# Kernel optimization log

Hardware: AMD Instinct MI355X
Metric: run time of the kernel (lower is better)

Reference implementation:

```python
import jax, jax.numpy as jnp
import numpy as np

N, E, G = 100000, 1600000, 8
IN, H, OUT = 3, 64, 20


def setup_inputs() -> dict:
    key = jax.random.key(0)
    ks = jax.random.split(key, 24)
    def nrm(k, shape, scale=0.1):
        return jax.random.normal(k, shape, dtype=jnp.float32) * scale
    inp = {}
    inp["x"] = jax.random.normal(ks[0], (N, IN), dtype=jnp.float32)
    inp["edge_index"] = jax.random.randint(ks[1], (2, E), 0, N, dtype=jnp.int32)
    inp["batch"] = jnp.sort(jax.random.randint(ks[2], (N,), 0, G, dtype=jnp.int32))
    dims = [(IN, H), (H, H), (H, H)]  # 3 GATConv layers (initial + layers-1)
    for i, (di, do) in enumerate(dims):
        inp[f"W{i}"] = nrm(ks[3 + 4 * i], (di, do))
        inp[f"as{i}"] = nrm(ks[4 + 4 * i], (do,))
        inp[f"ad{i}"] = nrm(ks[5 + 4 * i], (do,))
        inp[f"b{i}"] = jnp.zeros((do,), jnp.float32)
    inp["vn_emb0"] = jnp.zeros((1, H), jnp.float32)  # constant-0 init per module
    inp["m1_w1"] = nrm(ks[15], (H, H)); inp["m1_b1"] = jnp.zeros((H,), jnp.float32)
    inp["m1_w2"] = nrm(ks[16], (H, H)); inp["m1_b2"] = jnp.zeros((H,), jnp.float32)
    inp["mf_w1"] = nrm(ks[17], (H, H)); inp["mf_b1"] = jnp.zeros((H,), jnp.float32)
    inp["mf_w2"] = nrm(ks[18], (H, OUT)); inp["mf_b2"] = jnp.zeros((OUT,), jnp.float32)
    inp["out_w"] = nrm(ks[19], (H, OUT)); inp["out_b"] = jnp.zeros((OUT,), jnp.float32)
    return inp


def _gat(x, src, dst, W, a_s, a_d, b):
    # PyG GATConv, 1 head: h = xW; e_ij = LeakyReLU_0.2(a_s.h_j + a_d.h_i);
    # alpha = softmax over incoming edges of each dst node; out_i = sum_j alpha_ij h_j + b
    h = x @ W                                                  # [N, H]
    lg = jax.nn.leaky_relu((h @ a_s)[src] + (h @ a_d)[dst], 0.2)  # [E+N]
    m = jax.ops.segment_max(lg, dst, num_segments=N)
    m = jnp.where(jnp.isfinite(m), m, 0.0)
    p = jnp.exp(lg - m[dst])
    denom = jax.ops.segment_sum(p, dst, num_segments=N)
    alpha = p / denom[dst]
    return jax.ops.segment_sum(alpha[:, None] * h[src], dst, num_segments=N) + b


def _forward(x, edge_index, batch, params):
    (W0, as0, ad0, b0, W1, as1, ad1, b1, W2, as2, ad2, b2,
     vn_emb0, m1_w1, m1_b1, m1_w2, m1_b2, mf_w1, mf_b1, mf_w2, mf_b2,
     out_w, out_b) = params
    loops = jnp.arange(N, dtype=edge_index.dtype)  # GATConv add_self_loops=True
    src = jnp.concatenate([edge_index[0], loops])
    dst = jnp.concatenate([edge_index[1], loops])
    act = lambda v: jax.nn.leaky_relu(v, 0.01)  # nn.LeakyReLU default slope
    h = act(_gat(x, src, dst, W0, as0, ad0, b0))
    h = act(_gat(h, src, dst, W1, as1, ad1, b1))
    h = act(_gat(h, src, dst, W2, as2, ad2, b2))
    # virtual node: global_add_pool(out, batch) + Embedding(0) (zero-init)
    vn = jax.ops.segment_sum(h, batch, num_segments=G) + vn_emb0[0]
    vn = jax.nn.relu(vn @ m1_w1 + m1_b1)
    vn = jax.nn.relu(vn @ m1_w2 + m1_b2)
    vn = jax.nn.relu(vn @ mf_w1 + mf_b1)
    vn = jax.nn.relu(vn @ mf_w2 + mf_b2)
    return (h @ out_w + out_b, vn)


def reference(x, edge_index, batch, W0, as0, ad0, b0, W1, as1, ad1, b1,
              W2, as2, ad2, b2, vn_emb0, m1_w1, m1_b1, m1_w2, m1_b2,
              mf_w1, mf_b1, mf_w2, mf_b2, out_w, out_b):
    params = (W0, as0, ad0, b0, W1, as1, ad1, b1, W2, as2, ad2, b2,
              vn_emb0, m1_w1, m1_b1, m1_w2, m1_b2, mf_w1, mf_b1, mf_w2, mf_b2,
              out_w, out_b)
    return _forward(x, edge_index, batch, params)
```

## Files before the change

kernel.cpp:

```cpp
#include <hip/hip_runtime.h>
#include <hip/hip_bf16.h>

#define H 64
#define OUTD 20
#define NGRAPH 8
#define NBK 256
#define CAPB 8192
#define MAXDEG 63

typedef __attribute__((ext_vector_type(8))) short bf16x8;
typedef __attribute__((ext_vector_type(4))) float f32x4;
typedef __attribute__((ext_vector_type(8))) unsigned short u16x8;


__device__ __forceinline__ float ldp(const void* p, int i, bool f32) {
    return f32 ? ((const float*)p)[i]
               : __bfloat162float(((const __hip_bfloat16*)p)[i]);
}

__device__ __forceinline__ float bfu(unsigned short u) {
    union { unsigned int i; float f; } c; c.i = ((unsigned)u) << 16; return c.f;
}
__device__ __forceinline__ unsigned short fbits(float f) {
    __hip_bfloat16 b = __float2bfloat16(f);
    return *reinterpret_cast<unsigned short*>(&b);
}

__global__ void detect_dtype(const unsigned short* __restrict__ xb, int n_u16,
                             int* __restrict__ flag, int* __restrict__ gcur,
                             int* __restrict__ gtot, float* __restrict__ vnp,
                             float* __restrict__ s, short* __restrict__ hbuf,
                             int n, int ns) {
    __shared__ int sh[256];
    int t = threadIdx.x;
    int m = min(n_u16, 4096);
    int bad = 0;
    for (int i = t; i < m; i += 256) {
        unsigned e = (xb[i] >> 7) & 0xFF;
        bad += (e >= 0x90) ? 1 : 0;
    }
    sh[t] = bad;
    if (t < NBK) gcur[t] = 0;
    for (int i = t; i < NGRAPH * H; i += 256) vnp[i] = 0.f;
    if (t < 32) hbuf[(size_t)n * 32 + t] = 0;
    else if (t < 64) hbuf[((size_t)ns + n) * 32 + (t - 32)] = 0;
    if (t == 0) { *gtot = 0; s[n] = -1e30f; }
    __syncthreads();
    for (int off = 128; off; off >>= 1) {
        if (t < off) sh[t] += sh[t + off];
        __syncthreads();
    }
    if (t == 0) *flag = (sh[0] > (m >> 4)) ? 1 : 0;
}

__global__ void fillC_dense0(const int* __restrict__ src, const int* __restrict__ dst,
                             int* __restrict__ gcur, unsigned* __restrict__ ebuf,
                             int E, int n, int ns, int nC, int EPC, int nbk,
                             const void* __restrict__ x, const void* __restrict__ W,
                             const void* __restrict__ a_s, const void* __restrict__ a_d,
                             __hip_bfloat16* __restrict__ h, float* __restrict__ s,
                             float* __restrict__ d, const int* __restrict__ flagp) {
    if ((int)blockIdx.x < nC) {
        __shared__ unsigned lcnt[NBK];
        __shared__ int lbase[NBK];
        int t = threadIdx.x;
        for (int i = t; i < NBK; i += 256) lcnt[i] = 0;
        __syncthreads();
        int base = blockIdx.x * (256 * EPC) + t;
        for (int i = 0; i < EPC; ++i) {
            int e = base + i * 256;
            if (e < E) {
                int dn = dst[e];
                if ((unsigned)dn < (unsigned)n) atomicAdd(&lcnt[dn >> 9], 1u);
            }
        }
        __syncthreads();
        for (int i = t; i < nbk; i += 256) {
            unsigned c = lcnt[i];
            lbase[i] = c ? atomicAdd(&gcur[i], (int)c) : 0;
            lcnt[i] = 0;
        }
        __syncthreads();
        for (int i = 0; i < EPC; ++i) {
            int e = base + i * 256;
            if (e < E) {
                int dn = dst[e];
                if ((unsigned)dn < (unsigned)n) {
                    int b = dn >> 9;
                    unsigned pos = (unsigned)lbase[b] + atomicAdd(&lcnt[b], 1u);
                    if (pos < CAPB)
                        ebuf[(size_t)b * CAPB + pos] =
                            ((unsigned)src[e] << 9) | (unsigned)(dn & 511);
                }
            }
        }
        return;
    }
    const bool f32 = (*flagp != 0);
    int idx = ((int)blockIdx.x - nC) * 256 + threadIdx.x;
    int node = idx >> 6;
    int f = idx & 63;
    if (node >= n) return;
    float acc = 0.f;
    for (int k = 0; k < 3; ++k)
        acc += ldp(x, node * 3 + k, f32) * ldp(W, k * H + f, f32);
    ((short*)h)[((size_t)(f >> 5) * ns + node) * 32 + (f & 31)] = (short)fbits(acc);
    float sv = acc * ldp(a_s, f, f32);
    float dv = acc * ldp(a_d, f, f32);
    for (int off = 32; off; off >>= 1) {
        sv += __shfl_xor(sv, off);
        dv += __shfl_xor(dv, off);
    }
    if (f == 0) { s[node] = sv; d[node] = dv; }
}

__global__ __launch_bounds__(512) void bucketD(const unsigned* __restrict__ ebuf,
                                               const int* __restrict__ gcur,
                                               unsigned* __restrict__ cntoff,
                                               int* __restrict__ col,
                                               int* __restrict__ gtot, int n) {
    __shared__ unsigned lcnt[512];
    __shared__ int loff[512];
    __shared__ int sc[512];
    __shared__ int sdeg[512];
    __shared__ int sbase;
    int b = blockIdx.x, t = threadIdx.x;
    lcnt[t] = 0;
    __syncthreads();
    int end = min(gcur[b], CAPB);
    const unsigned* reg = ebuf + (size_t)b * CAPB;
    for (int i = t; i < end; i += 512) atomicAdd(&lcnt[reg[i] & 511u], 1u);
    __syncthreads();
    int node = (b << 9) + t;
    int degc = (node < n) ? (int)min(lcnt[t], (unsigned)MAXDEG) : 0;
    int d1 = degc + 1;
    int Dp = (node < n) ? ((d1 <= 24) ? ((d1 + 7) & ~7) : 64) : 0;
    sc[t] = Dp;
    __syncthreads();
    for (int ofs = 1; ofs < 512; ofs <<= 1) {
        int v = (t >= ofs) ? sc[t - ofs] : 0;
        __syncthreads();
        sc[t] += v;
        __syncthreads();
    }
    if (t == 511) sbase = atomicAdd(gtot, sc[511]);
    __syncthreads();
    int myoff = sbase + sc[t] - Dp;
    loff[t] = myoff;
    sdeg[t] = degc;
    if (node < n) cntoff[node] = (unsigned)myoff | ((unsigned)Dp << 24);
    lcnt[t] = 0;
    __syncthreads();
    int total = sc[511];
    for (int i = t; i < total; i += 512) col[sbase + i] = n;
    __syncthreads();
    if (node < n) col[myoff + degc] = node;
    for (int i = t; i < end; i += 512) {
        unsigned e = reg[i];
        int loc = (int)(e & 511u);
        unsigned pos = atomicAdd(&lcnt[loc], 1u);
        if ((int)pos < sdeg[loc])
            col[loff[loc] + pos] = (int)(e >> 9);
    }
}

#define ACC8(w, hv) { \
    a[0] += w * bfu(hv[0]); a[1] += w * bfu(hv[1]); \
    a[2] += w * bfu(hv[2]); a[3] += w * bfu(hv[3]); \
    a[4] += w * bfu(hv[4]); a[5] += w * bfu(hv[5]); \
    a[6] += w * bfu(hv[6]); a[7] += w * bfu(hv[7]); }

__global__ void gat_agg_sliced(const short* __restrict__ hs,
                               const float* __restrict__ s,
                               const float* __restrict__ d,
                               const unsigned* __restrict__ cntoff,
                               const int* __restrict__ col,
                               const void* __restrict__ bias,
                               short* __restrict__ outs, int n, int ns,
                               const int* __restrict__ flagp) {
    const bool f32 = (*flagp != 0);
    int shp = (int)blockIdx.x & 7;
    int fh = shp >> 2, nq = shp & 3;
    int qN = (n + 3) >> 2;
    int node = nq * qN + ((int)blockIdx.x >> 3) * 8 + ((int)threadIdx.x >> 5);
    int lim = min(n, (nq + 1) * qN);
    if (node >= lim) return;
    int l = threadIdx.x & 31;
    int c = l & 3, q = l >> 2;
    unsigned co = cntoff[node];
    int Dp = (int)(co >> 24);
    const int* cb = col + (co & 0xFFFFFFu);
    const char* hb = (const char*)hs + (size_t)fh * ns * 64;
    float di = d[node];
    unsigned coff = (unsigned)c * 16u;

    int s0 = cb[q];
    float v0 = s[s0] + di;
    u16x8 hv0 = *(const u16x8*)(hb + ((unsigned)s0 * 64u + coff));
    float sv0 = v0 > 0.f ? v0 : 0.2f * v0;

    float sv1 = -INFINITY, sv2 = -INFINITY;
    u16x8 hv1 = {}, hv2 = {};
    if (Dp > 8) {
        int s1 = cb[q + 8];
        float v1 = s[s1] + di;
        hv1 = *(const u16x8*)(hb + ((unsigned)s1 * 64u + coff));
        sv1 = v1 > 0.f ? v1 : 0.2f * v1;
    }
    if (Dp > 16) {
        int s2 = cb[q + 16];
        float v2 = s[s2] + di;
        hv2 = *(const u16x8*)(hb + ((unsigned)s2 * 64u + coff));
        sv2 = v2 > 0.f ? v2 : 0.2f * v2;
    }

    float sv3 = -INFINITY, sv4 = -INFINITY, sv5 = -INFINITY,
          sv6 = -INFINITY, sv7 = -INFINITY;
    u16x8 hv3 = {}, hv4 = {}, hv5 = {}, hv6 = {}, hv7 = {};
    bool big = (Dp > 24);
    if (big) {
        int s3 = cb[q + 24];
        int s4 = cb[q + 32];
        int s5 = cb[q + 40];
        int s6 = cb[q + 48];
        int s7 = cb[q + 56];
        float v3 = s[s3] + di, v4 = s[s4] + di, v5 = s[s5] + di,
              v6 = s[s6] + di, v7 = s[s7] + di;
        hv3 = *(const u16x8*)(hb + ((unsigned)s3 * 64u + coff));
        hv4 = *(const u16x8*)(hb + ((unsigned)s4 * 64u + coff));
        hv5 = *(const u16x8*)(hb + ((unsigned)s5 * 64u + coff));
        hv6 = *(const u16x8*)(hb + ((unsigned)s6 * 64u + coff));
        hv7 = *(const u16x8*)(hb + ((unsigned)s7 * 64u + coff));
        sv3 = v3 > 0.f ? v3 : 0.2f * v3;
        sv4 = v4 > 0.f ? v4 : 0.2f * v4;
        sv5 = v5 > 0.f ? v5 : 0.2f * v5;
        sv6 = v6 > 0.f ? v6 : 0.2f * v6;
        sv7 = v7 > 0.f ? v7 : 0.2f * v7;
    }

    float mx = fmaxf(fmaxf(fmaxf(sv0, sv1), fmaxf(sv2, sv3)),
                     fmaxf(fmaxf(sv4, sv5), fmaxf(sv6, sv7)));
    mx = fmaxf(mx, __shfl_xor(mx, 4));
    mx = fmaxf(mx, __shfl_xor(mx, 8));
    mx = fmaxf(mx, __shfl_xor(mx, 16));

    float w0 = __expf(sv0 - mx);
    float w1 = __expf(sv1 - mx);
    float w2 = __expf(sv2 - mx);
    float wsum = w0 + w1 + w2;

    float a[8] = {0.f, 0.f, 0.f, 0.f, 0.f, 0.f, 0.f, 0.f};
    ACC8(w0, hv0);
    ACC8(w1, hv1);
    ACC8(w2, hv2);
    if (big) {
        float w3 = __expf(sv3 - mx);
        float w4 = __expf(sv4 - mx);
        float w5 = __expf(sv5 - mx);
        float w6 = __expf(sv6 - mx);
        float w7 = __expf(sv7 - mx);
        wsum += w3 + w4 + w5 + w6 + w7;
        ACC8(w3, hv3);
        ACC8(w4, hv4);
        ACC8(w5, hv5);
        ACC8(w6, hv6);
        ACC8(w7, hv7);
    }
    wsum += __shfl_xor(wsum, 4);
    wsum += __shfl_xor(wsum, 8);
    wsum += __shfl_xor(wsum, 16);
#pragma unroll
    for (int i = 0; i < 8; ++i) {
        a[i] += __shfl_xor(a[i], 4);
        a[i] += __shfl_xor(a[i], 8);
        a[i] += __shfl_xor(a[i], 16);
    }
    if (q == 0) {
        float inv = 1.f / fmaxf(wsum, 1e-20f);
        u16x8 ov;
        for (int i = 0; i < 8; ++i) {
            float o = a[i] * inv + ldp(bias, fh * 32 + c * 8 + i, f32);
            o = o > 0.f ? o : 0.01f * o;
            ov[i] = fbits(o);
        }
        ((u16x8*)outs)[((size_t)fh * ns + node) * 4 + c] = ov;
    }
}


__global__ __launch_bounds__(256) void denseN_mfma(
    const __hip_bfloat16* __restrict__ in,
    const void* __restrict__ W,
    const void* __restrict__ a_s, const void* __restrict__ a_d,
    __hip_bfloat16* __restrict__ h, float* __restrict__ s,
    float* __restrict__ d, int n, int ns, const int* __restrict__ flagp) {
    const bool f32 = (*flagp != 0);
    __shared__ short Wt[64 * 72];
    int t = threadIdx.x;
    for (int i = t; i < 4096; i += 256) {
        int k = i >> 6, nf = i & 63;
        Wt[nf * 72 + k] = (short)fbits(ldp(W, i, f32));
    }
    __syncthreads();

    int wid = t >> 6, lane = t & 63;
    int quad = lane >> 4, n16 = lane & 15;
    int nodeBase = blockIdx.x * 64 + wid * 16;
    int mrow = nodeBase + n16;
    int mclamp = min(mrow, n - 1);
    const short* inp = (const short*)in;
    bf16x8 a0 = *(const bf16x8*)(inp + (size_t)mclamp * 32 + quad * 8);
    bf16x8 a1 = *(const bf16x8*)(inp + ((size_t)ns + mclamp) * 32 + quad * 8);

    float as_v[4], ad_v[4];
    for (int nt = 0; nt < 4; ++nt) {
        as_v[nt] = ldp(a_s, nt * 16 + n16, f32);
        ad_v[nt] = ldp(a_d, nt * 16 + n16, f32);
    }

    float sv[4] = {0.f, 0.f, 0.f, 0.f}, dv[4] = {0.f, 0.f, 0.f, 0.f};
    f32x4 accs[4];
    for (int nt = 0; nt < 4; ++nt) {
        const short* wrow = Wt + (nt * 16 + n16) * 72;
        bf16x8 b0 = *(const bf16x8*)(wrow + quad * 8);
        bf16x8 b1 = *(const bf16x8*)(wrow + 32 + quad * 8);
        f32x4 cacc = {0.f, 0.f, 0.f, 0.f};
        cacc = __builtin_amdgcn_mfma_f32_16x16x32_bf16(a0, b0, cacc, 0, 0, 0);
        cacc = __builtin_amdgcn_mfma_f32_16x16x32_bf16(a1, b1, cacc, 0, 0, 0);
        accs[nt] = cacc;
        for (int r = 0; r < 4; ++r) {
            sv[r] += cacc[r] * as_v[nt];
            dv[r] += cacc[r] * ad_v[nt];
        }
    }

    short* hb = (short*)h;
    for (int r = 0; r < 4; ++r) {
        int node = nodeBase + quad * 4 + r;
        if (node < n) {
            for (int nt = 0; nt < 4; ++nt) {
                int f = nt * 16 + n16;
                hb[((size_t)(f >> 5) * ns + node) * 32 + (f & 31)] = (short)fbits(accs[nt][r]);
            }
        }
    }
    for (int r = 0; r < 4; ++r) {
        for (int mask = 1; mask < 16; mask <<= 1) {
            sv[r] += __shfl_xor(sv[r], mask);
            dv[r] += __shfl_xor(dv[r], mask);
        }
    }
    if (n16 == 0) {
        for (int r = 0; r < 4; ++r) {
            int node = nodeBase + quad * 4 + r;
            if (node < n) { s[node] = sv[r]; d[node] = dv[r]; }
        }
    }
}


__global__ __launch_bounds__(256) void proj_pool(
    const __hip_bfloat16* __restrict__ h,
    const void* __restrict__ W, const void* __restrict__ b,
    void* __restrict__ out, int n, int ns, const int* __restrict__ flagp,
    int projBlocks, const int* __restrict__ batch, float* __restrict__ vn) {
    const bool f32 = (*flagp != 0);
    if ((int)blockIdx.x < projBlocks) {
        __shared__ short Wt[32 * 72];
        int t = threadIdx.x;
        for (int i = t; i < 32 * 64; i += 256) {
            int o = i >> 6, k = i & 63;
            Wt[o * 72 + k] = (o < OUTD) ? (short)fbits(ldp(W, k * OUTD + o, f32)) : 0;
        }
        __syncthreads();

        int wid = t >> 6, lane = t & 63;
        int quad = lane >> 4, n16 = lane & 15;
        int nodeBase = blockIdx.x * 64 + wid * 16;
        int mclamp = min(nodeBase + n16, n - 1);
        const short* hsrc = (const short*)h;
        bf16x8 a0 = *(const bf16x8*)(hsrc + (size_t)mclamp * 32 + quad * 8);
        bf16x8 a1 = *(const bf16x8*)(hsrc + ((size_t)ns + mclamp) * 32 + quad * 8);

        f32x4 acc0 = {0.f, 0.f, 0.f, 0.f}, acc1 = {0.f, 0.f, 0.f, 0.f};
        {
            const short* wrow = Wt + n16 * 72;
            bf16x8 b0 = *(const bf16x8*)(wrow + quad * 8);
            bf16x8 b1 = *(const bf16x8*)(wrow + 32 + quad * 8);
            acc0 = __builtin_amdgcn_mfma_f32_16x16x32_bf16(a0, b0, acc0, 0, 0, 0);
            acc0 = __builtin_amdgcn_mfma_f32_16x16x32_bf16(a1, b1, acc0, 0, 0, 0);
        }
        {
            const short* wrow = Wt + (16 + n16) * 72;
            bf16x8 b0 = *(const bf16x8*)(wrow + quad * 8);
            bf16x8 b1 = *(const bf16x8*)(wrow + 32 + quad * 8);
            acc1 = __builtin_amdgcn_mfma_f32_16x16x32_bf16(a0, b0, acc1, 0, 0, 0);
            acc1 = __builtin_amdgcn_mfma_f32_16x16x32_bf16(a1, b1, acc1, 0, 0, 0);
        }
        float bv0 = ldp(b, n16, f32);
        float bv1 = (n16 < OUTD - 16) ? ldp(b, 16 + n16, f32) : 0.f;
        for (int r = 0; r < 4; ++r) {
            int node = nodeBase + quad * 4 + r;
            if (node >= n) break;
            float o0 = acc0[r] + bv0;
            if (f32) ((float*)out)[node * OUTD + n16] = o0;
            else     ((__hip_bfloat16*)out)[node * OUTD + n16] = __float2bfloat16(o0);
            if (n16 < OUTD - 16) {
                float o1 = acc1[r] + bv1;
                if (f32) ((float*)out)[node * OUTD + 16 + n16] = o1;
                else     ((__hip_bfloat16*)out)[node * OUTD + 16 + n16] = __float2bfloat16(o1);
            }
        }
        return;
    }
    __shared__ float part[NGRAPH * H];
    int t = threadIdx.x;
    for (int i = t; i < NGRAPH * H; i += 256) part[i] = 0.f;
    __syncthreads();
    int pb = (int)blockIdx.x - projBlocks;
    int npb = gridDim.x - projBlocks;
    int wid = t >> 6, lane = t & 63;
    int gwave = pb * 4 + wid;
    int nwaves = npb * 4;
    int chunk = (n + nwaves - 1) / nwaves;
    int beg = gwave * chunk;
    int end = min(n, beg + chunk);
    if (beg < end) {
        const short* hb = (const short*)h + (size_t)(lane >> 5) * ns * 32 + (lane & 31);
        float acc = 0.f;
        int cur = batch[beg];
        for (int i = beg; i < end; ++i) {
            int g = batch[i];
            if (g != cur) {
                if ((unsigned)cur < NGRAPH) atomicAdd(&part[cur * H + lane], acc);
                acc = 0.f;
                cur = g;
            }
            acc += bfu((unsigned short)hb[(size_t)i * 32]);
        }
        if ((unsigned)cur < NGRAPH) atomicAdd(&part[cur * H + lane], acc);
    }
    __syncthreads();
    for (int i = t; i < NGRAPH * H; i += 256) {
        float v = part[i];
        if (v != 0.f) atomicAdd(&vn[i], v);
    }
}


__global__ void vn_mlp(const float* __restrict__ vn, const void* __restrict__ emb,
                       const void* __restrict__ w1, const void* __restrict__ b1,
                       const void* __restrict__ w2, const void* __restrict__ b2,
                       const void* __restrict__ w3, const void* __restrict__ b3,
                       const void* __restrict__ w4, const void* __restrict__ b4,
                       void* __restrict__ out, int out1_off, const int* __restrict__ flagp) {
    const bool f32 = (*flagp != 0);
    __shared__ float A[NGRAPH * H], B[NGRAPH * H];
    int t = threadIdx.x;
    int g = t >> 6, f = t & 63;
    A[t] = vn[t] + ldp(emb, f, f32);
    __syncthreads();
    float acc = ldp(b1, f, f32);
    for (int k = 0; k < H; ++k) acc += A[g * H + k] * ldp(w1, k * H + f, f32);
    B[t] = fmaxf(acc, 0.f);
    __syncthreads();
    acc = ldp(b2, f, f32);
    for (int k = 0; k < H; ++k) acc += B[g * H + k] * ldp(w2, k * H + f, f32);
    A[t] = fmaxf(acc, 0.f);
    __syncthreads();
    acc = ldp(b3, f, f32);
    for (int k = 0; k < H; ++k) acc += A[g * H + k] * ldp(w3, k * H + f, f32);
    B[t] = fmaxf(acc, 0.f);
    __syncthreads();
    if (f < OUTD) {
        acc = ldp(b4, f, f32);
        for (int k = 0; k < H; ++k) acc += B[g * H + k] * ldp(w4, k * OUTD + f, f32);
        acc = fmaxf(acc, 0.f);
        int idx = out1_off + g * OUTD + f;
        if (f32) ((float*)out)[idx] = acc;
        else     ((__hip_bfloat16*)out)[idx] = __float2bfloat16(acc);
    }
}


extern "C" void kernel_launch(void* const* d_in, const int* in_sizes, int n_in,
                              void* d_out, int out_size, void* d_ws, size_t ws_size,
                              hipStream_t stream) {
    const void* x   = d_in[0];
    const int* ei   = (const int*)d_in[1];
    const int* batch= (const int*)d_in[2];
    const void* W0  = d_in[3];
    const void* as0 = d_in[4];
    const void* ad0 = d_in[5];
    const void* b0  = d_in[6];
    const void* W1  = d_in[7];
    const void* as1 = d_in[8];
    const void* ad1 = d_in[9];
    const void* b1  = d_in[10];
    const void* W2  = d_in[11];
    const void* as2 = d_in[12];
    const void* ad2 = d_in[13];
    const void* b2  = d_in[14];
    const void* vne = d_in[15];
    const void* m1w1 = d_in[16];
    const void* m1b1 = d_in[17];
    const void* m1w2 = d_in[18];
    const void* m1b2 = d_in[19];
    const void* mfw1 = d_in[20];
    const void* mfb1 = d_in[21];
    const void* mfw2 = d_in[22];
    const void* mfb2 = d_in[23];
    const void* outw = d_in[24];
    const void* outb = d_in[25];

    const int N = in_sizes[2];
    const int E = in_sizes[1] / 2;
    const int NS = N + 1;
    const int* srcp = ei;
    const int* dstp = ei + E;

    char* w = (char*)d_ws;
    auto alloc = [&](size_t bytes) -> void* {
        void* p = (void*)w;
        w += ((bytes + 255) / 256) * 256;
        return p;
    };
    int*   flag   = (int*)alloc(256);
    int*   gcur   = (int*)alloc((size_t)NBK * 4);
    int*   gtot   = (int*)alloc(256);
    unsigned* ebuf= (unsigned*)alloc((size_t)NBK * CAPB * 4);
    unsigned* cntoff = (unsigned*)alloc((size_t)N * 4);
    int*   col    = (int*)alloc(((size_t)N * 64 + 64) * 4);
    __hip_bfloat16* featA = (__hip_bfloat16*)alloc((size_t)NS * H * 2);
    __hip_bfloat16* featB = (__hip_bfloat16*)alloc((size_t)NS * H * 2);
    __hip_bfloat16* hbuf  = (__hip_bfloat16*)alloc((size_t)NS * H * 2);
    float* sArr   = (float*)alloc((size_t)NS * 4);
    float* dArr   = (float*)alloc((size_t)N * 4);
    float* vn     = (float*)alloc((size_t)NGRAPH * H * 4);

    const int nbN64 = (N * H + 255) / 256;
    const int nb64 = (N + 63) / 64;
    const int projBlocks = (N + 63) / 64;
    const int nbk = (N + 511) >> 9;
    const int qN = (N + 3) >> 2;
    const int aggBlocks = 8 * ((qN + 7) / 8);
    int EPC = 8;
    int nC = (E + 256 * EPC - 1) / (256 * EPC);
    while (nC > 1024) { EPC <<= 1; nC = (E + 256 * EPC - 1) / (256 * EPC); }

    detect_dtype<<<1, 256, 0, stream>>>((const unsigned short*)x, in_sizes[0], flag,
                                        gcur, gtot, vn, sArr, (short*)hbuf, N, NS);

    fillC_dense0<<<nC + nbN64, 256, 0, stream>>>(
        srcp, dstp, gcur, ebuf, E, N, NS, nC, EPC, nbk,
        x, W0, as0, ad0, hbuf, sArr, dArr, flag);
    bucketD<<<nbk, 512, 0, stream>>>(ebuf, gcur, cntoff, col, gtot, N);

    gat_agg_sliced<<<aggBlocks, 256, 0, stream>>>((const short*)hbuf, sArr, dArr,
                                                  cntoff, col, b0, (short*)featA, N, NS, flag);
    denseN_mfma<<<nb64, 256, 0, stream>>>(featA, W1, as1, ad1, hbuf, sArr, dArr, N, NS, flag);
    gat_agg_sliced<<<aggBlocks, 256, 0, stream>>>((const short*)hbuf, sArr, dArr,
                                                  cntoff, col, b1, (short*)featB, N, NS, flag);
    denseN_mfma<<<nb64, 256, 0, stream>>>(featB, W2, as2, ad2, hbuf, sArr, dArr, N, NS, flag);
    gat_agg_sliced<<<aggBlocks, 256, 0, stream>>>((const short*)hbuf, sArr, dArr,
                                                  cntoff, col, b2, (short*)featA, N, NS, flag);

    proj_pool<<<projBlocks + 512, 256, 0, stream>>>(featA, outw, outb, d_out, N, NS, flag,
                                                    projBlocks, batch, vn);
    vn_mlp<<<1, 512, 0, stream>>>(vn, vne, m1w1, m1b1, m1w2, m1b2, mfw1, mfb1, mfw2, mfb2,
                                  d_out, N * OUTD, flag);
}
```

Before: 442.4 us.

## Pad small-degree rows to 24, use wave-shuffle scan, cache dst indices

Small-degree nodes now always get a padded row of 24 columns, so the aggregation kernel loads the first three neighbour groups unconditionally, with no divergent branches. The bucket kernel's block-wide prefix sum over shared memory with many barriers becomes a wave-level shuffle scan plus a short per-wave combine. The fill kernel keeps up to eight dst values in registers between its two passes so it does not re-read them from global memory. The cost is a larger column array and extra gathers of padding entries (pointing at node n) for low-degree nodes.

```diff
diff --git a/kernel.cpp b/kernel.cpp
--- a/kernel.cpp
+++ b/kernel.cpp
@@ -67,12 +67,12 @@
         for (int i = t; i < NBK; i += 256) lcnt[i] = 0;
         __syncthreads();
         int base = blockIdx.x * (256 * EPC) + t;
+        int dnr[8];
         for (int i = 0; i < EPC; ++i) {
             int e = base + i * 256;
-            if (e < E) {
-                int dn = dst[e];
-                if ((unsigned)dn < (unsigned)n) atomicAdd(&lcnt[dn >> 9], 1u);
-            }
+            int dn = (e < E) ? dst[e] : -1;
+            if (i < 8) dnr[i] = dn;
+            if ((unsigned)dn < (unsigned)n) atomicAdd(&lcnt[dn >> 9], 1u);
         }
         __syncthreads();
         for (int i = t; i < nbk; i += 256) {
@@ -84,7 +84,7 @@
         for (int i = 0; i < EPC; ++i) {
             int e = base + i * 256;
             if (e < E) {
-                int dn = dst[e];
+                int dn = (i < 8) ? dnr[i] : dst[e];
                 if ((unsigned)dn < (unsigned)n) {
                     int b = dn >> 9;
                     unsigned pos = (unsigned)lbase[b] + atomicAdd(&lcnt[b], 1u);
@@ -121,9 +121,9 @@
                                                int* __restrict__ gtot, int n) {
     __shared__ unsigned lcnt[512];
     __shared__ int loff[512];
-    __shared__ int sc[512];
     __shared__ int sdeg[512];
-    __shared__ int sbase;
+    __shared__ int wpart[8];
+    __shared__ int sbase, stot;
     int b = blockIdx.x, t = threadIdx.x;
     lcnt[t] = 0;
     __syncthreads();
@@ -133,25 +133,28 @@
     __syncthreads();
     int node = (b << 9) + t;
     int degc = (node < n) ? (int)min(lcnt[t], (unsigned)MAXDEG) : 0;
-    int d1 = degc + 1;
-    int Dp = (node < n) ? ((d1 <= 24) ? ((d1 + 7) & ~7) : 64) : 0;
-    sc[t] = Dp;
-    __syncthreads();
-    for (int ofs = 1; ofs < 512; ofs <<= 1) {
-        int v = (t >= ofs) ? sc[t - ofs] : 0;
-        __syncthreads();
-        sc[t] += v;
-        __syncthreads();
-    }
-    if (t == 511) sbase = atomicAdd(gtot, sc[511]);
-    __syncthreads();
-    int myoff = sbase + sc[t] - Dp;
+    int Dp = (node < n) ? ((degc + 1 <= 24) ? 24 : 64) : 0;
+    int lane = t & 63, wid = t >> 6;
+    int xs = Dp;
+    for (int o = 1; o < 64; o <<= 1) {
+        int v = __shfl_up(xs, o);
+        if (lane >= o) xs += v;
+    }
+    if (lane == 63) wpart[wid] = xs;
+    __syncthreads();
+    if (t == 0) {
+        int acc = 0;
+        for (int w8 = 0; w8 < 8; ++w8) { int v = wpart[w8]; wpart[w8] = acc; acc += v; }
+        stot = acc;
+        sbase = atomicAdd(gtot, acc);
+    }
+    __syncthreads();
+    int myoff = sbase + wpart[wid] + xs - Dp;
     loff[t] = myoff;
     sdeg[t] = degc;
     if (node < n) cntoff[node] = (unsigned)myoff | ((unsigned)Dp << 24);
     lcnt[t] = 0;
-    __syncthreads();
-    int total = sc[511];
+    int total = stot;
     for (int i = t; i < total; i += 512) col[sbase + i] = n;
     __syncthreads();
     if (node < n) col[myoff + degc] = node;
@@ -188,36 +191,26 @@
     int l = threadIdx.x & 31;
     int c = l & 3, q = l >> 2;
     unsigned co = cntoff[node];
-    int Dp = (int)(co >> 24);
+    bool big = (int)(co >> 24) > 24;
     const int* cb = col + (co & 0xFFFFFFu);
     const char* hb = (const char*)hs + (size_t)fh * ns * 64;
     float di = d[node];
     unsigned coff = (unsigned)c * 16u;
 
     int s0 = cb[q];
-    float v0 = s[s0] + di;
+    int s1 = cb[q + 8];
+    int s2 = cb[q + 16];
+    float v0 = s[s0] + di, v1 = s[s1] + di, v2 = s[s2] + di;
     u16x8 hv0 = *(const u16x8*)(hb + ((unsigned)s0 * 64u + coff));
+    u16x8 hv1 = *(const u16x8*)(hb + ((unsigned)s1 * 64u + coff));
+    u16x8 hv2 = *(const u16x8*)(hb + ((unsigned)s2 * 64u + coff));
     float sv0 = v0 > 0.f ? v0 : 0.2f * v0;
-
-    float sv1 = -INFINITY, sv2 = -INFINITY;
-    u16x8 hv1 = {}, hv2 = {};
-    if (Dp > 8) {
-        int s1 = cb[q + 8];
-        float v1 = s[s1] + di;
-        hv1 = *(const u16x8*)(hb + ((unsigned)s1 * 64u + coff));
-        sv1 = v1 > 0.f ? v1 : 0.2f * v1;
-    }
-    if (Dp > 16) {
-        int s2 = cb[q + 16];
-        float v2 = s[s2] + di;
-        hv2 = *(const u16x8*)(hb + ((unsigned)s2 * 64u + coff));
-        sv2 = v2 > 0.f ? v2 : 0.2f * v2;
-    }
+    float sv1 = v1 > 0.f ? v1 : 0.2f * v1;
+    float sv2 = v2 > 0.f ? v2 : 0.2f * v2;
 
     float sv3 = -INFINITY, sv4 = -INFINITY, sv5 = -INFINITY,
           sv6 = -INFINITY, sv7 = -INFINITY;
     u16x8 hv3 = {}, hv4 = {}, hv5 = {}, hv6 = {}, hv7 = {};
-    bool big = (Dp > 24);
     if (big) {
         int s3 = cb[q + 24];
         int s4 = cb[q + 32];
```

After: 427.2 us. -3.5%, faster.
